# Kernel optimization log

Measured on AMD Instinct MI355X. Metric: run time of the kernel, lower is better.

Reference implementation:

```python
import jax, jax.numpy as jnp
import numpy as np

B, N, P, K, C = 8, 4096, 4096, 32, 128  # batch, points, npoint, neighbors, channels (=mlp[-1])
W_OUT = 16  # weightnet output channels (from Linear(16*mlp[-1], mlp[-1]))
EPS = 1e-5


def setup_inputs() -> dict:
    key = jax.random.key(0)
    ks = jax.random.split(key, 9)
    xyz = jax.random.normal(ks[0], (B, P, 3), jnp.float32)
    points = jax.random.normal(ks[1], (B, N, C), jnp.float32)
    local_coordinates = jax.random.normal(ks[2], (B, P, K, 3), jnp.float32)
    neighbor_lists = jax.random.randint(ks[3], (B, P, K), 0, N)
    data_idx = jax.random.randint(ks[4], (B,), 0, B)
    Ww = jax.random.normal(ks[5], (3, W_OUT), jnp.float32) * 0.1   # weightnet (pointwise linear 3->16)
    bw = jnp.zeros((W_OUT,), jnp.float32)
    Wl = jax.random.normal(ks[6], (W_OUT * C, C), jnp.float32) * 0.02  # nn.Linear(16*mlp[-1], mlp[-1])
    bl = jnp.zeros((C,), jnp.float32)
    gamma = jnp.ones((C,), jnp.float32)   # BatchNorm1d weight
    beta = jnp.zeros((C,), jnp.float32)   # BatchNorm1d bias
    return {"xyz": xyz, "points": points, "local_coordinates": local_coordinates,
            "neighbor_lists": neighbor_lists, "data_idx": data_idx,
            "Ww": Ww, "bw": bw, "Wl": Wl, "bl": bl, "gamma": gamma, "beta": beta}


def reference(xyz, points, local_coordinates, neighbor_lists, data_idx, Ww, bw, Wl, bl, gamma, beta):
    b, p, k, _ = local_coordinates.shape
    c = points.shape[-1]
    # weightnet: pointwise map of 3-D local coordinates to 16 weight channels -> [B,P,K,16]
    weights = local_coordinates @ Ww + bw
    # irregular neighbor gather: data[b,p,k,:] = points[b, neighbor_lists[b,p,k], :] -> [B,P,K,C]
    data = points[jnp.arange(b)[:, None, None], neighbor_lists]
    # per-point weighted aggregation over K neighbors: [B,P,C,16] -> flatten to [B,P,C*16]
    new_points = jnp.einsum('bpkc,bpkw->bpcw', data, weights).reshape(b, p, c * weights.shape[-1])
    # batch reindex via data_idx
    new_points = new_points[data_idx]
    # linear tail: [B,P,C]
    new_points = new_points @ Wl + bl
    # BatchNorm1d over channel dim (training-mode batch stats), then ReLU: [B,C,P]
    x = new_points.transpose(0, 2, 1)
    mean = x.mean(axis=(0, 2), keepdims=True)
    var = x.var(axis=(0, 2), keepdims=True)
    x = (x - mean) * jax.lax.rsqrt(var + EPS) * gamma[None, :, None] + beta[None, :, None]
    return xyz, jax.nn.relu(x)
```

## Files before the change

kernel.cpp:

```cpp
#include <hip/hip_runtime.h>

#define Bn 8
#define Nn 4096
#define Pn 4096
#define Kn 32
#define Cn 128

using float4v = __attribute__((ext_vector_type(4))) float;
using short8  = __attribute__((ext_vector_type(8))) short;

__device__ __forceinline__ unsigned short bf16b(float f) {
  union { float f; unsigned u; } v; v.f = f;
  unsigned r = v.u + 0x7FFFu + ((v.u >> 16) & 1u);
  return (unsigned short)(r >> 16);
}

__device__ __forceinline__ unsigned pkhi(float x, float y) {
  return __builtin_amdgcn_perm(__float_as_uint(y), __float_as_uint(x), 0x07060302u);
}

__global__ __launch_bounds__(256) void prep(const float* __restrict__ Wl,
                                            unsigned short* __restrict__ WlT,
                                            const float* __restrict__ xyz,
                                            float* __restrict__ out,
                                            float* __restrict__ gacc) {
  __shared__ unsigned short tile[128 * 130];
  const int t = threadIdx.x, blk = blockIdx.x;
  if (blk < 16) {
#pragma unroll
    for (int i = 0; i < 64; ++i) {
      int idx = i * 256 + t;
      int kl = idx >> 7, n = idx & 127;
      tile[n * 130 + kl] = bf16b(Wl[(size_t)(blk * 128 + kl) * 128 + n]);
    }
    __syncthreads();
#pragma unroll
    for (int i = 0; i < 64; ++i) {
      int idx = i * 256 + t;
      int n = idx >> 7, kl = idx & 127;
      WlT[(size_t)n * 2048 + blk * 128 + kl] = tile[n * 130 + kl];
    }
  } else {
    if (blk == 16) gacc[t] = 0.f;
    const int i0 = (blk - 16) * 3072 + t * 12;
#pragma unroll
    for (int i = 0; i < 3; ++i)
      *(float4v*)(out + i0 + i * 4) = *(const float4v*)(xyz + i0 + i * 4);
  }
}

__global__ __launch_bounds__(256, 4) void fused(
    const float* __restrict__ points, const float* __restrict__ lc,
    const int* __restrict__ nl, const int* __restrict__ didx,
    const float* __restrict__ Ww, const float* __restrict__ bwv,
    const unsigned short* __restrict__ WlT, const float* __restrict__ blv,
    float* __restrict__ xout, float* __restrict__ gacc) {
  __shared__ unsigned short Mlds[32 * 256];
  __shared__ int nlds[32 * 32];
  __shared__ float red[256];

  const int t = threadIdx.x, lane = t & 63, w = t >> 6;
  const int l15 = lane & 15, q = lane >> 4;
  const int b = blockIdx.x & 7;
  const int pg = blockIdx.x >> 3;
  const int p0 = pg * 32;
  const int db = didx[b];
  const char* __restrict__ pbase = (const char*)(points + (size_t)db * Nn * Cn);

  const int* __restrict__ nlsrc = nl + (size_t)(db * Pn + p0) * Kn;
  *(int4*)&nlds[t * 4] = *(const int4*)(nlsrc + t * 4);

  const float Ww0 = Ww[l15], Ww1 = Ww[16 + l15], Ww2 = Ww[32 + l15];
  const float bw0 = bwv[l15];

  short8 af[8];
#pragma unroll
  for (int i = 0; i < 8; ++i) {
    const int p = p0 + w * 8 + i;
    const int pk = (db * Pn + p) * Kn;
    const float* __restrict__ lcp = lc + (size_t)(pk + q * 8) * 3;
    float la[24];
#pragma unroll
    for (int v = 0; v < 6; ++v) *(float4v*)&la[v * 4] = *(const float4v*)(lcp + v * 4);
#pragma unroll
    for (int j = 0; j < 8; ++j) {
      float ww = bw0 + la[3 * j] * Ww0 + la[3 * j + 1] * Ww1 + la[3 * j + 2] * Ww2;
      af[i][j] = (short)bf16b(ww);
    }
  }

  float4v acc[2][2];
#pragma unroll
  for (int pt = 0; pt < 2; ++pt)
#pragma unroll
    for (int nt = 0; nt < 2; ++nt) acc[pt][nt] = (float4v){0.f, 0.f, 0.f, 0.f};

  __syncthreads();

  const unsigned short* __restrict__ bpt =
      WlT + (size_t)(w * 32 + l15) * 2048 + q * 8;

  for (int ct = 0; ct < 8; ++ct) {
#pragma unroll
    for (int i = 0; i < 8; ++i) {
      const int pi = w * 8 + i;
      int nk[8];
      *(int4*)&nk[0] = *(const int4*)&nlds[pi * 32 + q * 8];
      *(int4*)&nk[4] = *(const int4*)&nlds[pi * 32 + q * 8 + 4];
      float f[8];
#pragma unroll
      for (int j = 0; j < 8; ++j)
        f[j] = *(const float*)(pbase +
                 (((unsigned)nk[j] << 9) + (unsigned)(l15 * 4 + ct * 64)));
      union { short8 s; unsigned u[4]; } bv;
#pragma unroll
      for (int i2 = 0; i2 < 4; ++i2) bv.u[i2] = pkhi(f[2 * i2], f[2 * i2 + 1]);
      float4v d = {0.f, 0.f, 0.f, 0.f};
      d = __builtin_amdgcn_mfma_f32_16x16x32_bf16(af[i], bv.s, d, 0, 0, 0);
      const unsigned off =
          (unsigned)(pi * 512 + ((l15 * 32 + q * 8) ^ ((pi & 7) << 4)));
      uint2 u;
      u.x = pkhi(d[0], d[1]);
      u.y = pkhi(d[2], d[3]);
      *(uint2*)((char*)Mlds + off) = u;
    }
    __syncthreads();
    const unsigned short* __restrict__ bp = bpt + ct * 256;
#pragma unroll
    for (int ks = 0; ks < 8; ++ks) {
      const unsigned ax = (unsigned)(ks * 64 + q * 16) ^ ((l15 & 7) << 4);
      short8 a0 = *(const short8*)((const char*)Mlds + l15 * 512 + ax);
      short8 a1 = *(const short8*)((const char*)Mlds + (16 + l15) * 512 + ax);
      short8 b0 = *(const short8*)(bp + ks * 32);
      short8 b1 = *(const short8*)(bp + 32768 + ks * 32);
      acc[0][0] = __builtin_amdgcn_mfma_f32_16x16x32_bf16(a0, b0, acc[0][0], 0, 0, 0);
      acc[0][1] = __builtin_amdgcn_mfma_f32_16x16x32_bf16(a0, b1, acc[0][1], 0, 0, 0);
      acc[1][0] = __builtin_amdgcn_mfma_f32_16x16x32_bf16(a1, b0, acc[1][0], 0, 0, 0);
      acc[1][1] = __builtin_amdgcn_mfma_f32_16x16x32_bf16(a1, b1, acc[1][1], 0, 0, 0);
    }
    __syncthreads();
  }

#pragma unroll
  for (int nt = 0; nt < 2; ++nt) {
    const int ch = w * 32 + nt * 16 + l15;
    const float bb = blv[ch];
    float s = 0.f, sq = 0.f;
#pragma unroll
    for (int pt = 0; pt < 2; ++pt) {
      float4v o;
#pragma unroll
      for (int r = 0; r < 4; ++r) {
        float v = acc[pt][nt][r] + bb; o[r] = v; s += v; sq += v * v;
      }
      *(float4v*)(xout + ((size_t)(b * Cn + ch)) * Pn + p0 + pt * 16 + q * 4) = o;
    }
    s += __shfl_xor(s, 16); s += __shfl_xor(s, 32);
    sq += __shfl_xor(sq, 16); sq += __shfl_xor(sq, 32);
    if (lane < 16) { red[ch] = s; red[128 + ch] = sq; }
  }
  __syncthreads();
  atomicAdd(&gacc[t], red[t]);
}

__global__ __launch_bounds__(256) void finalize_ln(float* __restrict__ x,
                                                   const float* __restrict__ gacc,
                                                   const float* __restrict__ gamma,
                                                   const float* __restrict__ beta) {
  const int idx = blockIdx.x * 256 + threadIdx.x;
  const int fi = idx * 4;
  const int c = (fi >> 12) & 127;
  const float inv = 1.f / 32768.f;
  const float mean = gacc[c] * inv;
  const float var = gacc[128 + c] * inv - mean * mean;
  const float scale = rsqrtf(var + 1e-5f) * gamma[c];
  const float shift = beta[c] - mean * scale;
  float4v v = *(float4v*)(x + fi);
#pragma unroll
  for (int r = 0; r < 4; ++r) v[r] = fmaxf(v[r] * scale + shift, 0.f);
  *(float4v*)(x + fi) = v;
}

extern "C" void kernel_launch(void* const* d_in, const int* in_sizes, int n_in,
                              void* d_out, int out_size, void* d_ws, size_t ws_size,
                              hipStream_t stream) {
  const float* xyz    = (const float*)d_in[0];
  const float* points = (const float*)d_in[1];
  const float* lc     = (const float*)d_in[2];
  const int*   nl     = (const int*)d_in[3];
  const int*   didx   = (const int*)d_in[4];
  const float* Ww     = (const float*)d_in[5];
  const float* bw     = (const float*)d_in[6];
  const float* Wl     = (const float*)d_in[7];
  const float* bl     = (const float*)d_in[8];
  const float* gamma  = (const float*)d_in[9];
  const float* beta   = (const float*)d_in[10];

  float* out  = (float*)d_out;
  float* xout = out + (size_t)Bn * Pn * 3;
  unsigned short* WlT = (unsigned short*)d_ws;
  float* gacc = (float*)((char*)d_ws + (size_t)512 * 1024);

  prep<<<48, 256, 0, stream>>>(Wl, WlT, xyz, out, gacc);
  fused<<<1024, 256, 0, stream>>>(points, lc, nl, didx, Ww, bw, WlT, bl,
                                  xout, gacc);
  finalize_ln<<<4096, 256, 0, stream>>>(xout, gacc, gamma, beta);
}
```

Measured before the change: 208.1 us.

## Double-buffer gather/MFMA pipeline with 64-point, 512-thread blocks

The fused kernel now processes 64 points per block with 8 waves and double-buffers the bf16 aggregation tile in LDS. The next channel-tile gather and its first MFMA stage are interleaved with the current tile's Wl MFMAs, using s_setprio to favor the matrix work. Each wave now owns 16 output channels across all 64 points, so each Wl fragment is reused four times. Neighbor indices are pre-shifted to byte offsets when staged into LDS. This targets the serialized gather-then-GEMM phases and the extra barrier, in exchange for more LDS (about 67 KB) and higher register pressure, which may limit occupancy.

```diff
diff --git a/kernel.cpp b/kernel.cpp
--- a/kernel.cpp
+++ b/kernel.cpp
@@ -49,26 +49,29 @@
   }
 }
 
-__global__ __launch_bounds__(256, 4) void fused(
+__global__ __launch_bounds__(512, 4) void fused(
     const float* __restrict__ points, const float* __restrict__ lc,
     const int* __restrict__ nl, const int* __restrict__ didx,
     const float* __restrict__ Ww, const float* __restrict__ bwv,
     const unsigned short* __restrict__ WlT, const float* __restrict__ blv,
     float* __restrict__ xout, float* __restrict__ gacc) {
-  __shared__ unsigned short Mlds[32 * 256];
-  __shared__ int nlds[32 * 32];
+  __shared__ unsigned short Mlds[2][64 * 256];
+  __shared__ int nlds[64 * 32];
   __shared__ float red[256];
 
   const int t = threadIdx.x, lane = t & 63, w = t >> 6;
   const int l15 = lane & 15, q = lane >> 4;
   const int b = blockIdx.x & 7;
   const int pg = blockIdx.x >> 3;
-  const int p0 = pg * 32;
+  const int p0 = pg * 64;
   const int db = didx[b];
   const char* __restrict__ pbase = (const char*)(points + (size_t)db * Nn * Cn);
 
-  const int* __restrict__ nlsrc = nl + (size_t)(db * Pn + p0) * Kn;
-  *(int4*)&nlds[t * 4] = *(const int4*)(nlsrc + t * 4);
+  {
+    int4 nv = *(const int4*)(nl + (size_t)(db * Pn + p0) * Kn + t * 4);
+    nv.x <<= 9; nv.y <<= 9; nv.z <<= 9; nv.w <<= 9;
+    *(int4*)&nlds[t * 4] = nv;
+  }
 
   const float Ww0 = Ww[l15], Ww1 = Ww[16 + l15], Ww2 = Ww[32 + l15];
   const float bw0 = bwv[l15];
@@ -89,78 +92,132 @@
     }
   }
 
-  float4v acc[2][2];
-#pragma unroll
-  for (int pt = 0; pt < 2; ++pt)
-#pragma unroll
-    for (int nt = 0; nt < 2; ++nt) acc[pt][nt] = (float4v){0.f, 0.f, 0.f, 0.f};
+  float4v acc[4];
+#pragma unroll
+  for (int rg = 0; rg < 4; ++rg) acc[rg] = (float4v){0.f, 0.f, 0.f, 0.f};
 
   __syncthreads();
 
-  const unsigned short* __restrict__ bpt =
-      WlT + (size_t)(w * 32 + l15) * 2048 + q * 8;
-
+  const unsigned short* __restrict__ bp =
+      WlT + (size_t)(w * 16 + l15) * 2048 + q * 8;
+  const unsigned cvoff = (unsigned)(l15 * 4);
+
+#define GATHER(i, ct, fdst)                                                \
+  {                                                                        \
+    const int pi_ = w * 8 + (i);                                           \
+    int nk_[8];                                                            \
+    *(int4*)&nk_[0] = *(const int4*)&nlds[pi_ * 32 + q * 8];               \
+    *(int4*)&nk_[4] = *(const int4*)&nlds[pi_ * 32 + q * 8 + 4];           \
+    _Pragma("unroll") for (int j = 0; j < 8; ++j)                          \
+        fdst[j] = *(const float*)(pbase + ((unsigned)nk_[j] + cvoff +      \
+                                           (unsigned)((ct) * 64)));        \
+  }
+
+#define FINISH(i, bsel, fsrc)                                              \
+  {                                                                        \
+    const int pi_ = w * 8 + (i);                                           \
+    union { short8 s; unsigned u[4]; } bv_;                                \
+    bv_.u[0] = pkhi(fsrc[0], fsrc[1]);                                     \
+    bv_.u[1] = pkhi(fsrc[2], fsrc[3]);                                     \
+    bv_.u[2] = pkhi(fsrc[4], fsrc[5]);                                     \
+    bv_.u[3] = pkhi(fsrc[6], fsrc[7]);                                     \
+    float4v d_ = {0.f, 0.f, 0.f, 0.f};                                     \
+    d_ = __builtin_amdgcn_mfma_f32_16x16x32_bf16(af[i], bv_.s, d_, 0, 0, 0); \
+    const unsigned off_ = (unsigned)((bsel) * 32768 + pi_ * 512 +          \
+        ((l15 * 32 + q * 8) ^ ((pi_ & 7) << 4)));                          \
+    uint2 u_;                                                              \
+    u_.x = pkhi(d_[0], d_[1]);                                             \
+    u_.y = pkhi(d_[2], d_[3]);                                             \
+    *(uint2*)((char*)Mlds + off_) = u_;                                    \
+  }
+
+#define STEP2KS(ks, bsel, bfrag)                                           \
+  {                                                                        \
+    const char* mb_ = (const char*)Mlds + (bsel) * 32768;                  \
+    const unsigned ax_ = (unsigned)(((ks) * 64 + q * 16) ^ ((l15 & 7) << 4)); \
+    short8 a0_ = *(const short8*)(mb_ + (l15) * 512 + ax_);                \
+    short8 a1_ = *(const short8*)(mb_ + (16 + l15) * 512 + ax_);           \
+    short8 a2_ = *(const short8*)(mb_ + (32 + l15) * 512 + ax_);           \
+    short8 a3_ = *(const short8*)(mb_ + (48 + l15) * 512 + ax_);           \
+    acc[0] = __builtin_amdgcn_mfma_f32_16x16x32_bf16(a0_, bfrag, acc[0], 0, 0, 0); \
+    acc[1] = __builtin_amdgcn_mfma_f32_16x16x32_bf16(a1_, bfrag, acc[1], 0, 0, 0); \
+    acc[2] = __builtin_amdgcn_mfma_f32_16x16x32_bf16(a2_, bfrag, acc[2], 0, 0, 0); \
+    acc[3] = __builtin_amdgcn_mfma_f32_16x16x32_bf16(a3_, bfrag, acc[3], 0, 0, 0); \
+  }
+
+  {
+    float f0[8][8];
+#pragma unroll
+    for (int i = 0; i < 8; ++i) GATHER(i, 0, f0[i])
+#pragma unroll
+    for (int i = 0; i < 8; ++i) FINISH(i, 0, f0[i])
+  }
+  __syncthreads();
+
+#pragma unroll
   for (int ct = 0; ct < 8; ++ct) {
-#pragma unroll
-    for (int i = 0; i < 8; ++i) {
-      const int pi = w * 8 + i;
-      int nk[8];
-      *(int4*)&nk[0] = *(const int4*)&nlds[pi * 32 + q * 8];
-      *(int4*)&nk[4] = *(const int4*)&nlds[pi * 32 + q * 8 + 4];
-      float f[8];
-#pragma unroll
-      for (int j = 0; j < 8; ++j)
-        f[j] = *(const float*)(pbase +
-                 (((unsigned)nk[j] << 9) + (unsigned)(l15 * 4 + ct * 64)));
-      union { short8 s; unsigned u[4]; } bv;
-#pragma unroll
-      for (int i2 = 0; i2 < 4; ++i2) bv.u[i2] = pkhi(f[2 * i2], f[2 * i2 + 1]);
-      float4v d = {0.f, 0.f, 0.f, 0.f};
-      d = __builtin_amdgcn_mfma_f32_16x16x32_bf16(af[i], bv.s, d, 0, 0, 0);
-      const unsigned off =
-          (unsigned)(pi * 512 + ((l15 * 32 + q * 8) ^ ((pi & 7) << 4)));
-      uint2 u;
-      u.x = pkhi(d[0], d[1]);
-      u.y = pkhi(d[2], d[3]);
-      *(uint2*)((char*)Mlds + off) = u;
+    const int cur = ct & 1, nxt = cur ^ 1;
+    short8 bqA[4];
+#pragma unroll
+    for (int ks = 0; ks < 4; ++ks)
+      bqA[ks] = *(const short8*)(bp + ct * 256 + ks * 32);
+    float fA[4][8];
+    if (ct < 7) {
+#pragma unroll
+      for (int i = 0; i < 4; ++i) GATHER(i, ct + 1, fA[i])
+    }
+    __builtin_amdgcn_s_setprio(1);
+    STEP2KS(0, cur, bqA[0])
+    STEP2KS(1, cur, bqA[1])
+    STEP2KS(2, cur, bqA[2])
+    STEP2KS(3, cur, bqA[3])
+    __builtin_amdgcn_s_setprio(0);
+    short8 bqB[4];
+#pragma unroll
+    for (int ks = 0; ks < 4; ++ks)
+      bqB[ks] = *(const short8*)(bp + ct * 256 + 128 + ks * 32);
+    float fB[4][8];
+    if (ct < 7) {
+#pragma unroll
+      for (int i = 0; i < 4; ++i) FINISH(i, nxt, fA[i])
+#pragma unroll
+      for (int i = 0; i < 4; ++i) GATHER(4 + i, ct + 1, fB[i])
+    }
+    __builtin_amdgcn_s_setprio(1);
+    STEP2KS(4, cur, bqB[0])
+    STEP2KS(5, cur, bqB[1])
+    STEP2KS(6, cur, bqB[2])
+    STEP2KS(7, cur, bqB[3])
+    __builtin_amdgcn_s_setprio(0);
+    if (ct < 7) {
+#pragma unroll
+      for (int i = 0; i < 4; ++i) FINISH(4 + i, nxt, fB[i])
     }
     __syncthreads();
-    const unsigned short* __restrict__ bp = bpt + ct * 256;
-#pragma unroll
-    for (int ks = 0; ks < 8; ++ks) {
-      const unsigned ax = (unsigned)(ks * 64 + q * 16) ^ ((l15 & 7) << 4);
-      short8 a0 = *(const short8*)((const char*)Mlds + l15 * 512 + ax);
-      short8 a1 = *(const short8*)((const char*)Mlds + (16 + l15) * 512 + ax);
-      short8 b0 = *(const short8*)(bp + ks * 32);
-      short8 b1 = *(const short8*)(bp + 32768 + ks * 32);
-      acc[0][0] = __builtin_amdgcn_mfma_f32_16x16x32_bf16(a0, b0, acc[0][0], 0, 0, 0);
-      acc[0][1] = __builtin_amdgcn_mfma_f32_16x16x32_bf16(a0, b1, acc[0][1], 0, 0, 0);
-      acc[1][0] = __builtin_amdgcn_mfma_f32_16x16x32_bf16(a1, b0, acc[1][0], 0, 0, 0);
-      acc[1][1] = __builtin_amdgcn_mfma_f32_16x16x32_bf16(a1, b1, acc[1][1], 0, 0, 0);
-    }
-    __syncthreads();
-  }
-
-#pragma unroll
-  for (int nt = 0; nt < 2; ++nt) {
-    const int ch = w * 32 + nt * 16 + l15;
+  }
+#undef GATHER
+#undef FINISH
+#undef STEP2KS
+
+  {
+    const int ch = w * 16 + l15;
     const float bb = blv[ch];
     float s = 0.f, sq = 0.f;
 #pragma unroll
-    for (int pt = 0; pt < 2; ++pt) {
+    for (int rg = 0; rg < 4; ++rg) {
       float4v o;
 #pragma unroll
       for (int r = 0; r < 4; ++r) {
-        float v = acc[pt][nt][r] + bb; o[r] = v; s += v; sq += v * v;
+        float v = acc[rg][r] + bb; o[r] = v; s += v; sq += v * v;
       }
-      *(float4v*)(xout + ((size_t)(b * Cn + ch)) * Pn + p0 + pt * 16 + q * 4) = o;
+      *(float4v*)(xout + ((size_t)(b * Cn + ch)) * Pn + p0 + rg * 16 + q * 4) = o;
     }
     s += __shfl_xor(s, 16); s += __shfl_xor(s, 32);
     sq += __shfl_xor(sq, 16); sq += __shfl_xor(sq, 32);
     if (lane < 16) { red[ch] = s; red[128 + ch] = sq; }
   }
   __syncthreads();
-  atomicAdd(&gacc[t], red[t]);
+  if (t < 256) atomicAdd(&gacc[t], red[t]);
 }
 
 __global__ __launch_bounds__(256) void finalize_ln(float* __restrict__ x,
@@ -202,7 +259,7 @@
   float* gacc = (float*)((char*)d_ws + (size_t)512 * 1024);
 
   prep<<<48, 256, 0, stream>>>(Wl, WlT, xyz, out, gacc);
-  fused<<<1024, 256, 0, stream>>>(points, lc, nl, didx, Ww, bw, WlT, bl,
-                                  xout, gacc);
+  fused<<<512, 512, 0, stream>>>(points, lc, nl, didx, Ww, bw, WlT, bl,
+                                 xout, gacc);
   finalize_ln<<<4096, 256, 0, stream>>>(xout, gacc, gamma, beta);
 }
```

After: 243.5 us. 17.0% more time.
